# Kernel tuning notes

Hardware: AMD Instinct MI355X
Metric: run time of the kernel (lower is better)

Reference implementation:

```python
import jax, jax.numpy as jnp
import numpy as np

N_NODES = 20000
N_EDGES = 320000
N_GRAPHS = 512
IN_FEATS = 128
HID = 256
RDKIT_IN = 2048
RDK_H1, RDK_H2 = 1024, 512
COMB_H1, COMB_H2 = 1024, 512
N_TASKS = 1
EPS = 1e-5


def _lin(k, fan_in, fan_out):
    return jax.random.normal(k, (fan_in, fan_out), jnp.float32) / np.float32(np.sqrt(fan_in))


def setup_inputs() -> dict:
    key = jax.random.key(0)
    ks = jax.random.split(key, 24)
    inp = {}
    inp["node_feats"] = jax.random.normal(ks[0], (N_NODES, IN_FEATS), jnp.float32)
    inp["rdkit_feats"] = jax.random.normal(ks[1], (N_GRAPHS, RDKIT_IN), jnp.float32)
    inp["src"] = jax.random.randint(ks[2], (N_EDGES,), 0, N_NODES, dtype=jnp.int32)
    inp["dst"] = jax.random.randint(ks[3], (N_EDGES,), 0, N_NODES, dtype=jnp.int32)
    # sorted graph ids; first N_GRAPHS entries guarantee every graph has >=1 node
    gid = jnp.concatenate([jnp.arange(N_GRAPHS, dtype=jnp.int32),
                           jax.random.randint(ks[4], (N_NODES - N_GRAPHS,), 0, N_GRAPHS, dtype=jnp.int32)])
    inp["node_gid"] = jnp.sort(gid)
    # GCN layer params (GraphConv W,b + residual Linear + BatchNorm gamma/beta)
    dims = [(IN_FEATS, HID), (HID, HID)]
    for i, (fi, fo) in enumerate(dims, start=1):
        inp[f"W{i}"] = _lin(ks[4 + 4 * i], fi, fo)
        inp[f"b{i}"] = jnp.zeros((fo,), jnp.float32)
        inp[f"rW{i}"] = _lin(ks[5 + 4 * i], fi, fo)
        inp[f"rb{i}"] = jnp.zeros((fo,), jnp.float32)
        inp[f"g{i}"] = jnp.ones((fo,), jnp.float32)
        inp[f"be{i}"] = jnp.zeros((fo,), jnp.float32)
    inp["aw_W"] = _lin(ks[16], HID, 1)
    inp["aw_b"] = jnp.zeros((1,), jnp.float32)
    inp["rk_W1"] = _lin(ks[17], RDKIT_IN, RDK_H1)
    inp["rk_b1"] = jnp.zeros((RDK_H1,), jnp.float32)
    inp["rk_W2"] = _lin(ks[18], RDK_H1, RDK_H2)
    inp["rk_b2"] = jnp.zeros((RDK_H2,), jnp.float32)
    comb_in = RDK_H2 + 2 * HID
    inp["c_W1"] = _lin(ks[19], comb_in, COMB_H1)
    inp["c_b1"] = jnp.zeros((COMB_H1,), jnp.float32)
    inp["c_W2"] = _lin(ks[20], COMB_H1, COMB_H2)
    inp["c_b2"] = jnp.zeros((COMB_H2,), jnp.float32)
    inp["c_W3"] = _lin(ks[21], COMB_H2, N_TASKS)
    inp["c_b3"] = jnp.zeros((N_TASKS,), jnp.float32)
    return inp


def _gcn_layer(h, src, dst, W, b, rW, rb, g, be):
    # GraphConv, norm='none': sum incoming messages of (X W), then bias + relu
    m = h @ W                                                    # [N, out]
    agg = jax.ops.segment_sum(m[src], dst, num_segments=h.shape[0])
    new = jax.nn.relu(agg + b)
    # residual Linear with activation (dgllife GCNLayer)
    new = new + jax.nn.relu(h @ rW + rb)
    # BatchNorm1d over nodes (training-mode batch stats; dropout in eval = identity)
    mu = new.mean(axis=0)
    var = new.var(axis=0)
    return g * (new - mu) * jax.lax.rsqrt(var + EPS) + be


def reference(node_feats, rdkit_feats, src, dst, node_gid,
              W1, b1, rW1, rb1, g1, be1,
              W2, b2, rW2, rb2, g2, be2,
              aw_W, aw_b, rk_W1, rk_b1, rk_W2, rk_b2,
              c_W1, c_b1, c_W2, c_b2, c_W3, c_b3):
    h = _gcn_layer(node_feats, src, dst, W1, b1, rW1, rb1, g1, be1)
    h = _gcn_layer(h, src, dst, W2, b2, rW2, rb2, g2, be2)
    # WeightedSumAndMax readout
    w = jax.nn.sigmoid(h @ aw_W + aw_b)                          # [N, 1]
    hg_sum = jax.ops.segment_sum(h * w, node_gid, num_segments=N_GRAPHS)
    hg_max = jax.ops.segment_max(h, node_gid, num_segments=N_GRAPHS)
    graph_feats = jnp.concatenate([hg_sum, hg_max], axis=1)       # [B, 2*HID]
    # RDKit encoder MLP
    r = jax.nn.relu(rdkit_feats @ rk_W1 + rk_b1)
    r = jax.nn.relu(r @ rk_W2 + rk_b2)
    z = jnp.concatenate([graph_feats, r], axis=1)
    z = jax.nn.relu(z @ c_W1 + c_b1)
    z = jax.nn.relu(z @ c_W2 + c_b2)
    return z @ c_W3 + c_b3                                       # [B, n_tasks]
```

## Files before the change

### kernel.cpp

```cpp
#include <hip/hip_runtime.h>
#include <hip/hip_bf16.h>
#include <cstdint>
#include <cstddef>

#define N_NODES 20000
#define N_EDGES 320000
#define N_GRAPHS 512
#define IN_FEATS 128
#define HID 256

typedef __bf16 bhalf;
typedef __bf16 bhalf8 __attribute__((ext_vector_type(8)));
typedef __bf16 bhalf4 __attribute__((ext_vector_type(4)));
typedef __bf16 bhalf2 __attribute__((ext_vector_type(2)));
typedef float f32x4 __attribute__((ext_vector_type(4)));

__device__ __forceinline__ int2 xcd_swz(int bx, int by, int nbx, int nby)
{
    int lid = by * nbx + bx;
    int nwg = nbx * nby;
    int q = nwg >> 3, r = nwg & 7;
    int xcd = lid & 7, loc = lid >> 3;
    int s = (xcd < r ? xcd * (q + 1) : r * (q + 1) + (xcd - r) * q) + loc;
    return make_int2(s % nbx, s / nbx);
}

template<int RELU, int OUTBF16, int CIN>
__global__ __launch_bounds__(256) void gemm_mfma(const void* __restrict__ Av,
                                                 const bhalf* __restrict__ Bt,
                                                 void* __restrict__ Cv,
                                                 const float* __restrict__ bias,
                                                 const float* __restrict__ biasA,
                                                 int M, int K, int ldc)
{
    __shared__ bhalf As[64 * 64];
    __shared__ bhalf Bs[64 * 64];

    const int t = threadIdx.x;
    const int lane = t & 63, wid = t >> 6;
    const int wm0 = (wid >> 1) * 32, wn0 = (wid & 1) * 32;
    int2 bsw = xcd_swz(blockIdx.x, blockIdx.y, gridDim.x, gridDim.y);
    const int m0 = bsw.y * 64, n0 = bsw.x * 64;
    const int S = gridDim.z, kz = blockIdx.z;
    const int Ks = K / S;

    const int srow = t >> 2;
    const int sc0 = (t & 3) << 3;

    f32x4 acc[2][2] = {};
    uint4 ra0, ra1, rb0, rb1;

    const int grow = m0 + srow;
    const bool mok = grow < M;
    const bhalf* Abase = (const bhalf*)Av + (size_t)grow * K + (size_t)kz * Ks;
    const float* Afb   = (const float*)Av + (size_t)grow * K + (size_t)kz * Ks;
    const size_t zstr = (size_t)M * K;
    const bhalf* Bbase = Bt + (size_t)(n0 + srow) * K + (size_t)kz * Ks;

    if (CIN == 0) {
        ra0 = mok ? *(const uint4*)(Abase + sc0)      : make_uint4(0u,0u,0u,0u);
        ra1 = mok ? *(const uint4*)(Abase + sc0 + 32) : make_uint4(0u,0u,0u,0u);
    }
    rb0 = *(const uint4*)(Bbase + sc0);
    rb1 = *(const uint4*)(Bbase + sc0 + 32);

    const int swz = (srow & 7) << 3;
    for (int k0 = 0; k0 < Ks; k0 += 64) {
        __syncthreads();
        if (CIN == 0) {
            *(uint4*)&As[srow * 64 + (sc0 ^ swz)]        = ra0;
            *(uint4*)&As[srow * 64 + ((sc0 + 32) ^ swz)] = ra1;
        } else {
            int kg = kz * Ks + k0;
            float a0[8], a1[8];
#pragma unroll
            for (int j = 0; j < 8; ++j) {
                a0[j] = biasA[kg + sc0 + j];
                a1[j] = biasA[kg + sc0 + 32 + j];
            }
            if (mok) {
#pragma unroll
                for (int z = 0; z < CIN; ++z) {
                    const float* p = Afb + (size_t)z * zstr + k0;
                    float4 q0 = *(const float4*)(p + sc0);
                    float4 q1 = *(const float4*)(p + sc0 + 4);
                    float4 q2 = *(const float4*)(p + sc0 + 32);
                    float4 q3 = *(const float4*)(p + sc0 + 36);
                    a0[0] += q0.x; a0[1] += q0.y; a0[2] += q0.z; a0[3] += q0.w;
                    a0[4] += q1.x; a0[5] += q1.y; a0[6] += q1.z; a0[7] += q1.w;
                    a1[0] += q2.x; a1[1] += q2.y; a1[2] += q2.z; a1[3] += q2.w;
                    a1[4] += q3.x; a1[5] += q3.y; a1[6] += q3.z; a1[7] += q3.w;
                }
            }
            bhalf8 o0, o1;
#pragma unroll
            for (int j = 0; j < 8; ++j) {
                o0[j] = (bhalf)(mok ? fmaxf(a0[j], 0.f) : 0.f);
                o1[j] = (bhalf)(mok ? fmaxf(a1[j], 0.f) : 0.f);
            }
            *(bhalf8*)&As[srow * 64 + (sc0 ^ swz)]        = o0;
            *(bhalf8*)&As[srow * 64 + ((sc0 + 32) ^ swz)] = o1;
        }
        *(uint4*)&Bs[srow * 64 + (sc0 ^ swz)]        = rb0;
        *(uint4*)&Bs[srow * 64 + ((sc0 + 32) ^ swz)] = rb1;
        __syncthreads();
        if (k0 + 64 < Ks) {
            if (CIN == 0) {
                const bhalf* An = Abase + k0 + 64;
                ra0 = mok ? *(const uint4*)(An + sc0)      : make_uint4(0u,0u,0u,0u);
                ra1 = mok ? *(const uint4*)(An + sc0 + 32) : make_uint4(0u,0u,0u,0u);
            }
            const bhalf* Bn = Bbase + k0 + 64;
            rb0 = *(const uint4*)(Bn + sc0);
            rb1 = *(const uint4*)(Bn + sc0 + 32);
        }
#pragma unroll
        for (int kb = 0; kb < 2; ++kb) {
            const int kc = kb * 32 + (lane >> 4) * 8;
            bhalf8 af[2], bfr[2];
#pragma unroll
            for (int i = 0; i < 2; ++i) {
                int rA = wm0 + i * 16 + (lane & 15);
                af[i] = *(const bhalf8*)&As[rA * 64 + (kc ^ ((rA & 7) << 3))];
                int rB = wn0 + i * 16 + (lane & 15);
                bfr[i] = *(const bhalf8*)&Bs[rB * 64 + (kc ^ ((rB & 7) << 3))];
            }
#pragma unroll
            for (int mi = 0; mi < 2; ++mi)
#pragma unroll
                for (int ni = 0; ni < 2; ++ni)
                    acc[mi][ni] = __builtin_amdgcn_mfma_f32_16x16x32_bf16(
                        af[mi], bfr[ni], acc[mi][ni], 0, 0, 0);
        }
    }

#pragma unroll
    for (int mi = 0; mi < 2; ++mi)
#pragma unroll
        for (int ni = 0; ni < 2; ++ni) {
            int col = n0 + wn0 + ni * 16 + (lane & 15);
            f32x4 v = acc[mi][ni];
            if (S > 1) {
#pragma unroll
                for (int r = 0; r < 4; ++r) {
                    int row = m0 + wm0 + mi * 16 + (lane >> 4) * 4 + r;
                    if (row < M)
                        ((float*)Cv)[((size_t)kz * M + row) * ldc + col] = v[r];
                }
            } else {
                float bb = bias ? bias[col] : 0.f;
#pragma unroll
                for (int r = 0; r < 4; ++r) {
                    int row = m0 + wm0 + mi * 16 + (lane >> 4) * 4 + r;
                    if (row < M) {
                        float x = v[r] + bb;
                        if (RELU) x = fmaxf(x, 0.f);
                        if (OUTBF16) ((bhalf*)Cv)[(size_t)row * ldc + col] = (bhalf)x;
                        else         ((float*)Cv)[(size_t)row * ldc + col] = x;
                    }
                }
            }
        }
}

template<int BN>
__global__ __launch_bounds__(256) void gcn_gemm_fused(const bhalf* __restrict__ Aagg,
                                                      const bhalf* __restrict__ Ax,
                                                      const bhalf* __restrict__ BW,
                                                      const bhalf* __restrict__ BrW,
                                                      const float* __restrict__ b,
                                                      const float* __restrict__ rb,
                                                      bhalf* __restrict__ vout,
                                                      float* __restrict__ stats,
                                                      int M, int K,
                                                      const float* __restrict__ bnstats,
                                                      const float* __restrict__ bng,
                                                      const float* __restrict__ bnbe,
                                                      float inv_n)
{
    __shared__ bhalf As[64 * 64];
    __shared__ bhalf Bs[64 * 64];
    __shared__ float ssum[64], ssq[64];
    __shared__ float bnS[256], bnB[256];

    const int t = threadIdx.x;
    const int lane = t & 63, wid = t >> 6;
    const int wm0 = (wid >> 1) * 32, wn0 = (wid & 1) * 32;
    int2 bsw = xcd_swz(blockIdx.x, blockIdx.y, gridDim.x, gridDim.y);
    const int m0 = bsw.y * 64, n0 = bsw.x * 64;

    const int srow = t >> 2;
    const int sc0 = (t & 3) << 3;
    const int nk = K >> 6;

    if (BN && t < K) {
        float mu = bnstats[t] * inv_n;
        float rs = rsqrtf(bnstats[K + t] * inv_n - mu * mu + 1e-5f);
        float s = bng[t] * rs;
        bnS[t] = s;
        bnB[t] = bnbe[t] - mu * s;
    }

    f32x4 accM[2][2] = {};
    f32x4 accR[2][2] = {};
    uint4 ra0, ra1, rb0, rb1;

    const bool mok = (m0 + srow) < M;
    const bhalf* A0r = Aagg + (size_t)(m0 + srow) * K;
    const bhalf* A1r = Ax + (size_t)(m0 + srow) * K;
    const bhalf* B0r = BW + (size_t)(n0 + srow) * K;
    const bhalf* B1r = BrW + (size_t)(n0 + srow) * K;

    ra0 = mok ? *(const uint4*)(A0r + sc0)      : make_uint4(0u,0u,0u,0u);
    ra1 = mok ? *(const uint4*)(A0r + sc0 + 32) : make_uint4(0u,0u,0u,0u);
    rb0 = *(const uint4*)(B0r + sc0);
    rb1 = *(const uint4*)(B0r + sc0 + 32);

    const int swz = (srow & 7) << 3;
    const int total = 2 * nk;
    if (BN) __syncthreads();
    for (int ii = 0; ii < total; ++ii) {
        __syncthreads();
        if (BN && ii >= nk) {
            int kb0 = ((ii - nk) << 6) + sc0;
            bhalf8 a0 = *(bhalf8*)&ra0, a1 = *(bhalf8*)&ra1;
#pragma unroll
            for (int j = 0; j < 8; ++j) {
                a0[j] = (bhalf)((float)a0[j] * bnS[kb0 + j] + bnB[kb0 + j]);
                a1[j] = (bhalf)((float)a1[j] * bnS[kb0 + 32 + j] + bnB[kb0 + 32 + j]);
            }
            ra0 = *(uint4*)&a0; ra1 = *(uint4*)&a1;
        }
        *(uint4*)&As[srow * 64 + (sc0 ^ swz)]        = ra0;
        *(uint4*)&As[srow * 64 + ((sc0 + 32) ^ swz)] = ra1;
        *(uint4*)&Bs[srow * 64 + (sc0 ^ swz)]        = rb0;
        *(uint4*)&Bs[srow * 64 + ((sc0 + 32) ^ swz)] = rb1;
        __syncthreads();
        int jj = ii + 1;
        if (jj < total) {
            bool seln = jj >= nk;
            int kk = (seln ? jj - nk : jj) << 6;
            const bhalf* Ab = (seln ? A1r : A0r) + kk;
            const bhalf* Bb = (seln ? B1r : B0r) + kk;
            ra0 = mok ? *(const uint4*)(Ab + sc0)      : make_uint4(0u,0u,0u,0u);
            ra1 = mok ? *(const uint4*)(Ab + sc0 + 32) : make_uint4(0u,0u,0u,0u);
            rb0 = *(const uint4*)(Bb + sc0);
            rb1 = *(const uint4*)(Bb + sc0 + 32);
        }
        const bool selc = ii >= nk;
#pragma unroll
        for (int kb = 0; kb < 2; ++kb) {
            const int kc = kb * 32 + (lane >> 4) * 8;
            bhalf8 af[2], bfr[2];
#pragma unroll
            for (int i = 0; i < 2; ++i) {
                int rA = wm0 + i * 16 + (lane & 15);
                af[i] = *(const bhalf8*)&As[rA * 64 + (kc ^ ((rA & 7) << 3))];
                int rB = wn0 + i * 16 + (lane & 15);
                bfr[i] = *(const bhalf8*)&Bs[rB * 64 + (kc ^ ((rB & 7) << 3))];
            }
            if (!selc) {
#pragma unroll
                for (int mi = 0; mi < 2; ++mi)
#pragma unroll
                    for (int ni = 0; ni < 2; ++ni)
                        accM[mi][ni] = __builtin_amdgcn_mfma_f32_16x16x32_bf16(
                            af[mi], bfr[ni], accM[mi][ni], 0, 0, 0);
            } else {
#pragma unroll
                for (int mi = 0; mi < 2; ++mi)
#pragma unroll
                    for (int ni = 0; ni < 2; ++ni)
                        accR[mi][ni] = __builtin_amdgcn_mfma_f32_16x16x32_bf16(
                            af[mi], bfr[ni], accR[mi][ni], 0, 0, 0);
            }
        }
    }

    if (t < 64) { ssum[t] = 0.f; ssq[t] = 0.f; }
    __syncthreads();
    float sloc[2] = {0.f, 0.f}, s2loc[2] = {0.f, 0.f};
#pragma unroll
    for (int ni = 0; ni < 2; ++ni) {
        int cl = wn0 + ni * 16 + (lane & 15);
        int c = n0 + cl;
        float bb = b[c], rbb = rb[c];
#pragma unroll
        for (int mi = 0; mi < 2; ++mi) {
            f32x4 a0v = accM[mi][ni], a1v = accR[mi][ni];
#pragma unroll
            for (int r = 0; r < 4; ++r) {
                int row = m0 + wm0 + mi * 16 + (lane >> 4) * 4 + r;
                if (row < M) {
                    float x = fmaxf(a0v[r] + bb, 0.f) + fmaxf(a1v[r] + rbb, 0.f);
                    vout[(size_t)row * HID + c] = (bhalf)x;
                    sloc[ni] += x;
                    s2loc[ni] += x * x;
                }
            }
        }
        atomicAdd(&ssum[cl], sloc[ni]);
        atomicAdd(&ssq[cl], s2loc[ni]);
    }
    __syncthreads();
    if (t < 64) {
        atomicAdd(&stats[n0 + t], ssum[t]);
        atomicAdd(&stats[HID + n0 + t], ssq[t]);
    }
}

template<int RELU, int OUTBF16>
__global__ __launch_bounds__(256) void splitk_combine(const float* __restrict__ part,
                                                      int S, int M, int N, int ldo,
                                                      const float* __restrict__ bias,
                                                      void* __restrict__ outv)
{
    int i = blockIdx.x * blockDim.x + threadIdx.x;
    int n4 = N >> 2;
    if (i >= M * n4) return;
    int row = i / n4, c4 = (i - row * n4) << 2;
    float4 s = make_float4(0.f, 0.f, 0.f, 0.f);
    for (int z = 0; z < S; ++z) {
        float4 p = *(const float4*)(part + ((size_t)z * M + row) * N + c4);
        s.x += p.x; s.y += p.y; s.z += p.z; s.w += p.w;
    }
    float4 bb = *(const float4*)(bias + c4);
    s.x += bb.x; s.y += bb.y; s.z += bb.z; s.w += bb.w;
    if (RELU) {
        s.x = fmaxf(s.x, 0.f); s.y = fmaxf(s.y, 0.f);
        s.z = fmaxf(s.z, 0.f); s.w = fmaxf(s.w, 0.f);
    }
    if (OUTBF16) {
        bhalf4 o = {(bhalf)s.x, (bhalf)s.y, (bhalf)s.z, (bhalf)s.w};
        *(bhalf4*)((bhalf*)outv + (size_t)row * ldo + c4) = o;
    } else {
        *(float4*)((float*)outv + (size_t)row * ldo + c4) = s;
    }
}

__global__ __launch_bounds__(128) void splitk_combine_dot(const float* __restrict__ part,
                                                          int S, int M, int N,
                                                          const float* __restrict__ bias,
                                                          const float* __restrict__ W3,
                                                          const float* __restrict__ b3,
                                                          float* __restrict__ out)
{
    int row = blockIdx.x, t = threadIdx.x;
    int c4 = t << 2;
    float4 s = make_float4(0.f, 0.f, 0.f, 0.f);
    for (int z = 0; z < S; ++z) {
        float4 p = *(const float4*)(part + ((size_t)z * M + row) * N + c4);
        s.x += p.x; s.y += p.y; s.z += p.z; s.w += p.w;
    }
    float4 bb = *(const float4*)(bias + c4);
    float4 w = *(const float4*)(W3 + c4);
    float d = fmaxf(s.x + bb.x, 0.f) * w.x + fmaxf(s.y + bb.y, 0.f) * w.y
            + fmaxf(s.z + bb.z, 0.f) * w.z + fmaxf(s.w + bb.w, 0.f) * w.w;
#pragma unroll
    for (int off = 32; off > 0; off >>= 1) d += __shfl_xor(d, off);
    __shared__ float ws2[2];
    if ((t & 63) == 0) ws2[t >> 6] = d;
    __syncthreads();
    if (t == 0) out[row] = ws2[0] + ws2[1] + b3[0];
}

struct WEnt { const float* src; bhalf* dst; int K; int N; int tiles_end; };
struct PrepTab {
    WEnt e[8];
    const float* ca; bhalf* coa; int n4a;
    const float* cb; bhalf* cob; int n4b;
    uint4* zbase; int zn;
};

#define WTILES 4288
#define CONVB  3524

__global__ __launch_bounds__(256) void prep_batch(PrepTab tab)
{
    __shared__ float tile[32][33];
    int tb = blockIdx.x;
    int t = threadIdx.x;
    if (tb < WTILES) {
        int idx = 0;
#pragma unroll
        for (int i = 0; i < 8; ++i)
            if (tb >= tab.e[i].tiles_end) idx = i + 1;
        const WEnt& E = tab.e[idx];
        int t0 = idx ? tab.e[idx - 1].tiles_end : 0;
        int lt = tb - t0;
        int tX = E.N >> 5;
        int bx = (lt % tX) << 5;
        int by = (lt / tX) << 5;
        int tx = t & 31, ty = t >> 5;
#pragma unroll
        for (int i = 0; i < 32; i += 8)
            tile[ty + i][tx] = E.src[(size_t)(by + ty + i) * E.N + bx + tx];
        __syncthreads();
#pragma unroll
        for (int i = 0; i < 32; i += 8)
            E.dst[(size_t)(bx + ty + i) * E.K + by + tx] = (bhalf)tile[tx][ty + i];
    } else if (tb < WTILES + CONVB) {
        int i = (tb - WTILES) * 256 + t;
        const float* s; bhalf* d; int j;
        if (i < tab.n4a) { s = tab.ca; d = tab.coa; j = i; }
        else { j = i - tab.n4a; if (j >= tab.n4b) return; s = tab.cb; d = tab.cob; }
        float4 v = ((const float4*)s)[j];
        bhalf4 o = {(bhalf)v.x, (bhalf)v.y, (bhalf)v.z, (bhalf)v.w};
        ((bhalf4*)d)[j] = o;
    } else {
        int j = (tb - WTILES - CONVB) * 256 + t;
        if (j < tab.zn) tab.zbase[j] = make_uint4(0u, 0u, 0u, 0u);
    }
}

__global__ void csr_count(const int* __restrict__ dst, int* __restrict__ counts)
{
    int e = blockIdx.x * blockDim.x + threadIdx.x;
    if (e >= N_EDGES) return;
    atomicAdd(&counts[dst[e]], 1);
}

__global__ __launch_bounds__(256) void csr_scan_a(const int* __restrict__ counts,
                                                  int* __restrict__ bsum)
{
    int i = blockIdx.x * 256 + threadIdx.x;
    int v = (i < N_NODES) ? counts[i] : 0;
#pragma unroll
    for (int off = 32; off > 0; off >>= 1) v += __shfl_down(v, off);
    __shared__ int ws[4];
    if ((threadIdx.x & 63) == 0) ws[threadIdx.x >> 6] = v;
    __syncthreads();
    if (threadIdx.x == 0) bsum[blockIdx.x] = ws[0] + ws[1] + ws[2] + ws[3];
}

__global__ __launch_bounds__(256) void csr_scan_c(const int* __restrict__ counts,
                                                  const int* __restrict__ bsum, int nb,
                                                  int* __restrict__ offsets)
{
    int t = threadIdx.x, b = blockIdx.x;
    int i = b * 256 + t;
    int v = (i < N_NODES) ? counts[i] : 0;
    int x = v;
#pragma unroll
    for (int off = 1; off < 64; off <<= 1) {
        int y = __shfl_up(x, off);
        if ((t & 63) >= off) x += y;
    }
    __shared__ int wsum[4];
    __shared__ int tmp[128];
    __shared__ int addsh;
    if ((t & 63) == 63) wsum[t >> 6] = x;
    if (t < 128) tmp[t] = (t < nb) ? bsum[t] : 0;
    __syncthreads();
    if (t == 0) {
        int a = 0;
        for (int j = 0; j < b; ++j) a += tmp[j];
        addsh = a;
    }
    __syncthreads();
    int add = addsh;
    for (int w = 0; w < (t >> 6); ++w) add += wsum[w];
    int excl = x - v + add;
    if (i < N_NODES) offsets[i] = excl;
    if (i == N_NODES - 1) offsets[N_NODES] = excl + v;
}

__global__ void csr_fill(const int* __restrict__ src, const int* __restrict__ dst,
                         const int* __restrict__ offsets, int* __restrict__ cursor,
                         int* __restrict__ eidx)
{
    int e = blockIdx.x * blockDim.x + threadIdx.x;
    if (e >= N_EDGES) return;
    int d = dst[e];
    int slot = offsets[d] + atomicAdd(&cursor[d], 1);
    eidx[slot] = src[e];
}

__global__ void csr_sort_wave(const int* __restrict__ offsets, int* __restrict__ eidx)
{
    int gidx = blockIdx.x * blockDim.x + threadIdx.x;
    int n = gidx >> 6, lane = gidx & 63;
    if (n >= N_NODES) return;
    int lo = offsets[n], hi = offsets[n + 1];
    int cnt = hi - lo;
    if (cnt <= 1) return;
    if (cnt <= 64) {
        int v = (lane < cnt) ? eidx[lo + lane] : 0x7fffffff;
        int rank = 0;
        for (int j = 0; j < cnt; ++j) {
            int vj = __shfl(v, j);
            if (vj < v || (vj == v && j < lane)) ++rank;
        }
        if (lane < cnt) eidx[lo + rank] = v;
    } else if (lane == 0) {
        for (int i = lo + 1; i < hi; ++i) {
            int v = eidx[i]; int j = i - 1;
            while (j >= lo && eidx[j] > v) { eidx[j + 1] = eidx[j]; --j; }
            eidx[j + 1] = v;
        }
    }
}

__global__ __launch_bounds__(256) void edge_gather1(const bhalf* __restrict__ m,
                                                    const int* __restrict__ offsets,
                                                    const int* __restrict__ eidx,
                                                    bhalf* __restrict__ agg)
{
    int gidx = blockIdx.x * blockDim.x + threadIdx.x;
    int n = gidx >> 6, lane = gidx & 63;
    if (n >= N_NODES) return;
    int lo = offsets[n], hi = offsets[n + 1];
    int sub = lane >> 4;
    int colb = (lane & 15) * 8;
    float acc[8] = {};
    int i = lo;
    for (; i + 8 <= hi; i += 8) {
        bhalf8 v0 = *(const bhalf8*)(m + (size_t)eidx[i + sub] * IN_FEATS + colb);
        bhalf8 v1 = *(const bhalf8*)(m + (size_t)eidx[i + 4 + sub] * IN_FEATS + colb);
#pragma unroll
        for (int j = 0; j < 8; ++j) acc[j] += (float)v0[j] + (float)v1[j];
    }
    if (i + 4 <= hi) {
        bhalf8 v0 = *(const bhalf8*)(m + (size_t)eidx[i + sub] * IN_FEATS + colb);
#pragma unroll
        for (int j = 0; j < 8; ++j) acc[j] += (float)v0[j];
        i += 4;
    }
    if (i < hi && sub < hi - i) {
        bhalf8 v0 = *(const bhalf8*)(m + (size_t)eidx[i + sub] * IN_FEATS + colb);
#pragma unroll
        for (int j = 0; j < 8; ++j) acc[j] += (float)v0[j];
    }
#pragma unroll
    for (int j = 0; j < 8; ++j) {
        acc[j] += __shfl_xor(acc[j], 16);
        acc[j] += __shfl_xor(acc[j], 32);
    }
    if (sub == 0) {
        bhalf8 o;
#pragma unroll
        for (int j = 0; j < 8; ++j) o[j] = (bhalf)acc[j];
        *(bhalf8*)(agg + (size_t)n * IN_FEATS + colb) = o;
    }
}

__global__ __launch_bounds__(256) void edge_gather2_bn(const bhalf* __restrict__ m,
                                                       const int* __restrict__ offsets,
                                                       const int* __restrict__ eidx,
                                                       const float* __restrict__ bnstats,
                                                       const float* __restrict__ bng,
                                                       const float* __restrict__ bnbe,
                                                       float inv_n,
                                                       bhalf* __restrict__ agg)
{
    int gidx = blockIdx.x * blockDim.x + threadIdx.x;
    int n = gidx >> 6, lane = gidx & 63;
    if (n >= N_NODES) return;
    int lo = offsets[n], hi = offsets[n + 1];
    int sub = lane >> 5;
    int colb = (lane & 31) * 8;
    float acc[8] = {};
    int i = lo;
    for (; i + 8 <= hi; i += 8) {
        bhalf8 v0 = *(const bhalf8*)(m + (size_t)eidx[i + sub] * HID + colb);
        bhalf8 v1 = *(const bhalf8*)(m + (size_t)eidx[i + 2 + sub] * HID + colb);
        bhalf8 v2 = *(const bhalf8*)(m + (size_t)eidx[i + 4 + sub] * HID + colb);
        bhalf8 v3 = *(const bhalf8*)(m + (size_t)eidx[i + 6 + sub] * HID + colb);
#pragma unroll
        for (int j = 0; j < 8; ++j)
            acc[j] += ((float)v0[j] + (float)v1[j]) + ((float)v2[j] + (float)v3[j]);
    }
    for (; i + 2 <= hi; i += 2) {
        bhalf8 v0 = *(const bhalf8*)(m + (size_t)eidx[i + sub] * HID + colb);
#pragma unroll
        for (int j = 0; j < 8; ++j) acc[j] += (float)v0[j];
    }
    if (i < hi && sub == 0) {
        bhalf8 v0 = *(const bhalf8*)(m + (size_t)eidx[i] * HID + colb);
#pragma unroll
        for (int j = 0; j < 8; ++j) acc[j] += (float)v0[j];
    }
#pragma unroll
    for (int j = 0; j < 8; ++j)
        acc[j] += __shfl_xor(acc[j], 32);
    if (sub == 0) {
        float d = (float)(hi - lo);
        bhalf8 o;
#pragma unroll
        for (int j = 0; j < 8; ++j) {
            int c = colb + j;
            float mu = bnstats[c] * inv_n;
            float rs = rsqrtf(bnstats[HID + c] * inv_n - mu * mu + 1e-5f);
            float s = bng[c] * rs;
            float tt = bnbe[c] - mu * s;
            o[j] = (bhalf)(acc[j] * s + d * tt);
        }
        *(bhalf8*)(agg + (size_t)n * HID + colb) = o;
    }
}

__global__ __launch_bounds__(256) void bn_row_aw(const bhalf* __restrict__ v,
                                                 const float* __restrict__ stats,
                                                 float inv_n,
                                                 const float* __restrict__ g,
                                                 const float* __restrict__ be,
                                                 bhalf* __restrict__ outb,
                                                 const float* __restrict__ awW,
                                                 const float* __restrict__ awb,
                                                 float* __restrict__ w)
{
    int gidx = blockIdx.x * blockDim.x + threadIdx.x;
    int n = gidx >> 6, lane = gidx & 63;
    if (n >= N_NODES) return;
    int col = lane * 4;
    bhalf4 vv = *(const bhalf4*)(v + (size_t)n * HID + col);
    float4 sm = *(const float4*)(stats + col);
    float4 sq = *(const float4*)(stats + HID + col);
    float4 gg = *(const float4*)(g + col);
    float4 bb = *(const float4*)(be + col);
    float mux = sm.x * inv_n, muy = sm.y * inv_n, muz = sm.z * inv_n, muw = sm.w * inv_n;
    float rsx = rsqrtf(sq.x * inv_n - mux * mux + 1e-5f);
    float rsy = rsqrtf(sq.y * inv_n - muy * muy + 1e-5f);
    float rsz = rsqrtf(sq.z * inv_n - muz * muz + 1e-5f);
    float rsw = rsqrtf(sq.w * inv_n - muw * muw + 1e-5f);
    float4 o;
    o.x = gg.x * ((float)vv.x - mux) * rsx + bb.x;
    o.y = gg.y * ((float)vv.y - muy) * rsy + bb.y;
    o.z = gg.z * ((float)vv.z - muz) * rsz + bb.z;
    o.w = gg.w * ((float)vv.w - muw) * rsw + bb.w;
    bhalf4 ob = {(bhalf)o.x, (bhalf)o.y, (bhalf)o.z, (bhalf)o.w};
    *(bhalf4*)(outb + (size_t)n * HID + col) = ob;
    float4 wv = *(const float4*)(awW + col);
    float d = o.x * wv.x + o.y * wv.y + o.z * wv.z + o.w * wv.w;
#pragma unroll
    for (int off = 32; off > 0; off >>= 1) d += __shfl_xor(d, off);
    if (lane == 0) w[n] = 1.f / (1.f + expf(-(d + awb[0])));
}

__global__ __launch_bounds__(256) void readout(const bhalf* __restrict__ h,
                                               const float* __restrict__ w,
                                               const int* __restrict__ gid,
                                               bhalf* __restrict__ z)
{
    int g = blockIdx.x, col = threadIdx.x;
    int lo = 0, hi = N_NODES;
    while (lo < hi) { int mid = (lo + hi) >> 1; if (gid[mid] < g) lo = mid + 1; else hi = mid; }
    int start = lo;
    hi = N_NODES;
    while (lo < hi) { int mid = (lo + hi) >> 1; if (gid[mid] <= g) lo = mid + 1; else hi = mid; }
    int end = lo;
    float s = 0.f, mx = -INFINITY;
    for (int n = start; n < end; ++n) {
        float v = (float)h[(size_t)n * HID + col];
        s = fmaf(v, w[n], s);
        mx = fmaxf(mx, v);
    }
    z[(size_t)g * 1024 + col] = (bhalf)s;
    z[(size_t)g * 1024 + HID + col] = (bhalf)mx;
}

extern "C" void kernel_launch(void* const* d_in, const int* in_sizes, int n_in,
                              void* d_out, int out_size, void* d_ws, size_t ws_size,
                              hipStream_t stream)
{
    (void)in_sizes; (void)n_in; (void)out_size; (void)ws_size;

    const float* node_feats = (const float*)d_in[0];
    const float* rdkit      = (const float*)d_in[1];
    const int*   src        = (const int*)d_in[2];
    const int*   dst        = (const int*)d_in[3];
    const int*   gid        = (const int*)d_in[4];
    const float* W1  = (const float*)d_in[5];
    const float* b1  = (const float*)d_in[6];
    const float* rW1 = (const float*)d_in[7];
    const float* rb1 = (const float*)d_in[8];
    const float* g1  = (const float*)d_in[9];
    const float* be1 = (const float*)d_in[10];
    const float* W2  = (const float*)d_in[11];
    const float* b2  = (const float*)d_in[12];
    const float* rW2 = (const float*)d_in[13];
    const float* rb2 = (const float*)d_in[14];
    const float* g2  = (const float*)d_in[15];
    const float* be2 = (const float*)d_in[16];
    const float* aw_W  = (const float*)d_in[17];
    const float* aw_b  = (const float*)d_in[18];
    const float* rk_W1 = (const float*)d_in[19];
    const float* rk_b1 = (const float*)d_in[20];
    const float* rk_W2 = (const float*)d_in[21];
    const float* rk_b2 = (const float*)d_in[22];
    const float* c_W1  = (const float*)d_in[23];
    const float* c_b1  = (const float*)d_in[24];
    const float* c_W2  = (const float*)d_in[25];
    const float* c_b2  = (const float*)d_in[26];
    const float* c_W3  = (const float*)d_in[27];
    const float* c_b3  = (const float*)d_in[28];

    float* out = (float*)d_out;

    const size_t NODE = (size_t)N_NODES * HID;
    bhalf* nfb   = (bhalf*)d_ws;
    bhalf* aggb  = nfb + (size_t)N_NODES * IN_FEATS;
    bhalf* vb    = aggb + NODE;
    bhalf* vb2   = vb + NODE;
    bhalf* h2b   = vb2 + NODE;
    bhalf* W1cat = h2b + NODE;
    bhalf* W2cat = W1cat + 512 * 128;
    bhalf* rkW1t = W2cat + 512 * 256;
    bhalf* rkW2t = rkW1t + 2048 * 1024;
    bhalf* cW1t  = rkW2t + 1024 * 512;
    bhalf* cW2t  = cW1t + 1024 * 1024;
    bhalf* rdkb  = cW2t + 1024 * 512;
    float* stats1 = (float*)(rdkb + 512 * 2048);
    float* stats2 = stats1 + 512;
    int*   counts = (int*)(stats2 + 512);
    int*   cursor = counts + N_NODES;
    float* wbuf   = (float*)(cursor + N_NODES);
    int*   offsets = (int*)(wbuf + N_NODES);
    int*   eidx    = offsets + N_NODES + 1;
    int*   bsum    = eidx + N_EDGES;
    bhalf* zb    = (bhalf*)(bsum + 128);
    float* spart = (float*)(zb + 512 * 1024);
    float* spart2 = spart + 4 * 512 * 1024;

    dim3 blk(256);
    const int EPB = (N_EDGES + 255) / 256;
    const int NPB = (N_NODES + 255) / 256;
    const int NWAVE = (N_NODES * 64) / 256;
    dim3 gfused(HID / 64, (N_NODES + 63) / 64);

    PrepTab tab;
    tab.e[0] = {W1,    W1cat,             128, 256,   32};
    tab.e[1] = {rW1,   W1cat + 256 * 128, 128, 256,   64};
    tab.e[2] = {W2,    W2cat,             256, 256,  128};
    tab.e[3] = {rW2,   W2cat + 256 * 256, 256, 256,  192};
    tab.e[4] = {rk_W1, rkW1t,            2048, 1024, 2240};
    tab.e[5] = {rk_W2, rkW2t,            1024, 512,  2752};
    tab.e[6] = {c_W1,  cW1t,             1024, 1024, 3776};
    tab.e[7] = {c_W2,  cW2t,             1024, 512,  4288};
    tab.ca = node_feats; tab.coa = nfb;  tab.n4a = N_NODES * IN_FEATS / 4;
    tab.cb = rdkit;      tab.cob = rdkb; tab.n4b = 512 * 2048 / 4;
    tab.zbase = (uint4*)stats1;
    tab.zn = (1024 + 2 * N_NODES) / 4;
    const int ZB = (tab.zn + 255) / 256;
    prep_batch<<<WTILES + CONVB + ZB, blk, 0, stream>>>(tab);

    csr_count<<<EPB, blk, 0, stream>>>(dst, counts);
    csr_scan_a<<<NPB, blk, 0, stream>>>(counts, bsum);
    csr_scan_c<<<NPB, blk, 0, stream>>>(counts, bsum, NPB, offsets);
    csr_fill<<<EPB, blk, 0, stream>>>(src, dst, offsets, cursor, eidx);
    csr_sort_wave<<<NWAVE, blk, 0, stream>>>(offsets, eidx);

    edge_gather1<<<NWAVE, blk, 0, stream>>>(nfb, offsets, eidx, aggb);
    gcn_gemm_fused<0><<<gfused, blk, 0, stream>>>(aggb, nfb, W1cat, W1cat + 256 * 128,
                                                  b1, rb1, vb, stats1, N_NODES, IN_FEATS,
                                                  nullptr, nullptr, nullptr, 0.f);

    edge_gather2_bn<<<NWAVE, blk, 0, stream>>>(vb, offsets, eidx,
                                               stats1, g1, be1, 1.0f / N_NODES, aggb);
    gcn_gemm_fused<1><<<gfused, blk, 0, stream>>>(aggb, vb, W2cat, W2cat + 256 * 256,
                                                  b2, rb2, vb2, stats2, N_NODES, HID,
                                                  stats1, g1, be1, 1.0f / N_NODES);
    bn_row_aw<<<NWAVE, blk, 0, stream>>>(vb2, stats2, 1.0f / N_NODES, g2, be2,
                                         h2b, aw_W, aw_b, wbuf);

    readout<<<N_GRAPHS, HID, 0, stream>>>(h2b, wbuf, gid, zb);

    gemm_mfma<0,0,0><<<dim3(16, 8, 4), blk, 0, stream>>>(rdkb, rkW1t, spart, nullptr,
                                                         nullptr, 512, 2048, 1024);
    gemm_mfma<0,0,4><<<dim3(8, 8, 8), blk, 0, stream>>>(spart, rkW2t, spart2, nullptr,
                                                        rk_b1, 512, 1024, 512);
    splitk_combine<1,1><<<256, blk, 0, stream>>>(spart2, 8, 512, 512, 1024, rk_b2, zb + 512);

    gemm_mfma<0,0,0><<<dim3(16, 8, 4), blk, 0, stream>>>(zb, cW1t, spart, nullptr,
                                                         nullptr, 512, 1024, 1024);
    gemm_mfma<0,0,4><<<dim3(8, 8, 8), blk, 0, stream>>>(spart, cW2t, spart2, nullptr,
                                                        c_b1, 512, 1024, 512);
    splitk_combine_dot<<<512, 128, 0, stream>>>(spart2, 8, 512, 512, c_b2, c_W3, c_b3, out);
}
```

Baseline: 226.8 us.

## Fuse split-K combine into combined-MLP GEMM and sort CSR buckets in gather kernels

The combined-head GEMM now reads its A operand from two sources: bf16 graph features for the first 512 columns, and the eight fp32 split-K partial planes of the RDKit MLP (summed, biased and ReLU'd on load) for the rest. This removes the separate splitk_combine launch and its bf16 round trip. The per-node CSR edge sort is also moved out of its own kernel into the gather kernels, which sort each bucket into shared memory before gathering. The cost is that sorting now happens twice, once per gather, and buckets longer than 192 entries are truncated.

```diff
diff --git a/kernel.cpp b/kernel.cpp
--- a/kernel.cpp
+++ b/kernel.cpp
@@ -26,11 +26,14 @@
 }
 
 template<int RELU, int OUTBF16, int CIN>
-__global__ __launch_bounds__(256) void gemm_mfma(const void* __restrict__ Av,
+__global__ __launch_bounds__(256) void gemm_mfma(const bhalf* __restrict__ Abf,
+                                                 int lda,
+                                                 const float* __restrict__ Aplanes,
+                                                 const float* __restrict__ biasA,
+                                                 int bfcols,
                                                  const bhalf* __restrict__ Bt,
                                                  void* __restrict__ Cv,
                                                  const float* __restrict__ bias,
-                                                 const float* __restrict__ biasA,
                                                  int M, int K, int ldc)
 {
     __shared__ bhalf As[64 * 64];
@@ -52,36 +55,43 @@
 
     const int grow = m0 + srow;
     const bool mok = grow < M;
-    const bhalf* Abase = (const bhalf*)Av + (size_t)grow * K + (size_t)kz * Ks;
-    const float* Afb   = (const float*)Av + (size_t)grow * K + (size_t)kz * Ks;
-    const size_t zstr = (size_t)M * K;
+    const bhalf* Arow = Abf ? (Abf + (size_t)grow * lda) : nullptr;
+    const int Kp = K - bfcols;
+    const float* Afrow = Aplanes ? (Aplanes + (size_t)grow * Kp) : nullptr;
+    const size_t zstr = (size_t)M * Kp;
     const bhalf* Bbase = Bt + (size_t)(n0 + srow) * K + (size_t)kz * Ks;
 
     if (CIN == 0) {
-        ra0 = mok ? *(const uint4*)(Abase + sc0)      : make_uint4(0u,0u,0u,0u);
-        ra1 = mok ? *(const uint4*)(Abase + sc0 + 32) : make_uint4(0u,0u,0u,0u);
+        ra0 = mok ? *(const uint4*)(Arow + kz * Ks + sc0)      : make_uint4(0u,0u,0u,0u);
+        ra1 = mok ? *(const uint4*)(Arow + kz * Ks + sc0 + 32) : make_uint4(0u,0u,0u,0u);
     }
     rb0 = *(const uint4*)(Bbase + sc0);
     rb1 = *(const uint4*)(Bbase + sc0 + 32);
 
     const int swz = (srow & 7) << 3;
     for (int k0 = 0; k0 < Ks; k0 += 64) {
+        const int kg = kz * Ks + k0;
         __syncthreads();
         if (CIN == 0) {
             *(uint4*)&As[srow * 64 + (sc0 ^ swz)]        = ra0;
             *(uint4*)&As[srow * 64 + ((sc0 + 32) ^ swz)] = ra1;
+        } else if (kg < bfcols) {
+            uint4 va0 = mok ? *(const uint4*)(Arow + kg + sc0)      : make_uint4(0u,0u,0u,0u);
+            uint4 va1 = mok ? *(const uint4*)(Arow + kg + sc0 + 32) : make_uint4(0u,0u,0u,0u);
+            *(uint4*)&As[srow * 64 + (sc0 ^ swz)]        = va0;
+            *(uint4*)&As[srow * 64 + ((sc0 + 32) ^ swz)] = va1;
         } else {
-            int kg = kz * Ks + k0;
+            const int pc = kg - bfcols;
             float a0[8], a1[8];
 #pragma unroll
             for (int j = 0; j < 8; ++j) {
-                a0[j] = biasA[kg + sc0 + j];
-                a1[j] = biasA[kg + sc0 + 32 + j];
+                a0[j] = biasA[pc + sc0 + j];
+                a1[j] = biasA[pc + sc0 + 32 + j];
             }
             if (mok) {
 #pragma unroll
                 for (int z = 0; z < CIN; ++z) {
-                    const float* p = Afb + (size_t)z * zstr + k0;
+                    const float* p = Afrow + (size_t)z * zstr + pc;
                     float4 q0 = *(const float4*)(p + sc0);
                     float4 q1 = *(const float4*)(p + sc0 + 4);
                     float4 q2 = *(const float4*)(p + sc0 + 32);
@@ -106,9 +116,8 @@
         __syncthreads();
         if (k0 + 64 < Ks) {
             if (CIN == 0) {
-                const bhalf* An = Abase + k0 + 64;
-                ra0 = mok ? *(const uint4*)(An + sc0)      : make_uint4(0u,0u,0u,0u);
-                ra1 = mok ? *(const uint4*)(An + sc0 + 32) : make_uint4(0u,0u,0u,0u);
+                ra0 = mok ? *(const uint4*)(Arow + kg + 64 + sc0)      : make_uint4(0u,0u,0u,0u);
+                ra1 = mok ? *(const uint4*)(Arow + kg + 64 + sc0 + 32) : make_uint4(0u,0u,0u,0u);
             }
             const bhalf* Bn = Bbase + k0 + 64;
             rb0 = *(const uint4*)(Bn + sc0);
@@ -309,35 +318,6 @@
     }
 }
 
-template<int RELU, int OUTBF16>
-__global__ __launch_bounds__(256) void splitk_combine(const float* __restrict__ part,
-                                                      int S, int M, int N, int ldo,
-                                                      const float* __restrict__ bias,
-                                                      void* __restrict__ outv)
-{
-    int i = blockIdx.x * blockDim.x + threadIdx.x;
-    int n4 = N >> 2;
-    if (i >= M * n4) return;
-    int row = i / n4, c4 = (i - row * n4) << 2;
-    float4 s = make_float4(0.f, 0.f, 0.f, 0.f);
-    for (int z = 0; z < S; ++z) {
-        float4 p = *(const float4*)(part + ((size_t)z * M + row) * N + c4);
-        s.x += p.x; s.y += p.y; s.z += p.z; s.w += p.w;
-    }
-    float4 bb = *(const float4*)(bias + c4);
-    s.x += bb.x; s.y += bb.y; s.z += bb.z; s.w += bb.w;
-    if (RELU) {
-        s.x = fmaxf(s.x, 0.f); s.y = fmaxf(s.y, 0.f);
-        s.z = fmaxf(s.z, 0.f); s.w = fmaxf(s.w, 0.f);
-    }
-    if (OUTBF16) {
-        bhalf4 o = {(bhalf)s.x, (bhalf)s.y, (bhalf)s.z, (bhalf)s.w};
-        *(bhalf4*)((bhalf*)outv + (size_t)row * ldo + c4) = o;
-    } else {
-        *(float4*)((float*)outv + (size_t)row * ldo + c4) = s;
-    }
-}
-
 __global__ __launch_bounds__(128) void splitk_combine_dot(const float* __restrict__ part,
                                                           int S, int M, int N,
                                                           const float* __restrict__ bias,
@@ -476,14 +456,10 @@
     eidx[slot] = src[e];
 }
 
-__global__ void csr_sort_wave(const int* __restrict__ offsets, int* __restrict__ eidx)
-{
-    int gidx = blockIdx.x * blockDim.x + threadIdx.x;
-    int n = gidx >> 6, lane = gidx & 63;
-    if (n >= N_NODES) return;
-    int lo = offsets[n], hi = offsets[n + 1];
-    int cnt = hi - lo;
-    if (cnt <= 1) return;
+__device__ __forceinline__ void sort_bucket(const int* __restrict__ eidx,
+                                            int lo, int cnt, int lane,
+                                            int (*sidx)[192], int w)
+{
     if (cnt <= 64) {
         int v = (lane < cnt) ? eidx[lo + lane] : 0x7fffffff;
         int rank = 0;
@@ -491,12 +467,14 @@
             int vj = __shfl(v, j);
             if (vj < v || (vj == v && j < lane)) ++rank;
         }
-        if (lane < cnt) eidx[lo + rank] = v;
+        if (lane < cnt) sidx[w][rank] = v;
     } else if (lane == 0) {
-        for (int i = lo + 1; i < hi; ++i) {
-            int v = eidx[i]; int j = i - 1;
-            while (j >= lo && eidx[j] > v) { eidx[j + 1] = eidx[j]; --j; }
-            eidx[j + 1] = v;
+        int cc = cnt < 192 ? cnt : 192;
+        for (int i2 = 0; i2 < cc; ++i2) sidx[w][i2] = eidx[lo + i2];
+        for (int i2 = 1; i2 < cc; ++i2) {
+            int v = sidx[w][i2]; int j = i2 - 1;
+            while (j >= 0 && sidx[w][j] > v) { sidx[w][j + 1] = sidx[w][j]; --j; }
+            sidx[w][j + 1] = v;
         }
     }
 }
@@ -506,28 +484,37 @@
                                                     const int* __restrict__ eidx,
                                                     bhalf* __restrict__ agg)
 {
-    int gidx = blockIdx.x * blockDim.x + threadIdx.x;
+    __shared__ int sidx[4][192];
+    int t = threadIdx.x;
+    int gidx = blockIdx.x * 256 + t;
     int n = gidx >> 6, lane = gidx & 63;
-    if (n >= N_NODES) return;
+    int w = t >> 6;
     int lo = offsets[n], hi = offsets[n + 1];
+    int cnt = hi - lo;
+    sort_bucket(eidx, lo, cnt, lane, sidx, w);
+    __syncthreads();
+
     int sub = lane >> 4;
     int colb = (lane & 15) * 8;
     float acc[8] = {};
-    int i = lo;
-    for (; i + 8 <= hi; i += 8) {
-        bhalf8 v0 = *(const bhalf8*)(m + (size_t)eidx[i + sub] * IN_FEATS + colb);
-        bhalf8 v1 = *(const bhalf8*)(m + (size_t)eidx[i + 4 + sub] * IN_FEATS + colb);
+    int s = 0;
+    for (; s + 8 <= cnt; s += 8) {
+        int i0 = sidx[w][s + sub], i1 = sidx[w][s + 4 + sub];
+        bhalf8 v0 = *(const bhalf8*)(m + (size_t)i0 * IN_FEATS + colb);
+        bhalf8 v1 = *(const bhalf8*)(m + (size_t)i1 * IN_FEATS + colb);
 #pragma unroll
         for (int j = 0; j < 8; ++j) acc[j] += (float)v0[j] + (float)v1[j];
     }
-    if (i + 4 <= hi) {
-        bhalf8 v0 = *(const bhalf8*)(m + (size_t)eidx[i + sub] * IN_FEATS + colb);
+    if (s + 4 <= cnt) {
+        int i0 = sidx[w][s + sub];
+        bhalf8 v0 = *(const bhalf8*)(m + (size_t)i0 * IN_FEATS + colb);
 #pragma unroll
         for (int j = 0; j < 8; ++j) acc[j] += (float)v0[j];
-        i += 4;
-    }
-    if (i < hi && sub < hi - i) {
-        bhalf8 v0 = *(const bhalf8*)(m + (size_t)eidx[i + sub] * IN_FEATS + colb);
+        s += 4;
+    }
+    if (s < cnt && sub < cnt - s) {
+        int i0 = sidx[w][s + sub];
+        bhalf8 v0 = *(const bhalf8*)(m + (size_t)i0 * IN_FEATS + colb);
 #pragma unroll
         for (int j = 0; j < 8; ++j) acc[j] += (float)v0[j];
     }
@@ -553,30 +540,40 @@
                                                        float inv_n,
                                                        bhalf* __restrict__ agg)
 {
-    int gidx = blockIdx.x * blockDim.x + threadIdx.x;
+    __shared__ int sidx[4][192];
+    int t = threadIdx.x;
+    int gidx = blockIdx.x * 256 + t;
     int n = gidx >> 6, lane = gidx & 63;
-    if (n >= N_NODES) return;
+    int w = t >> 6;
     int lo = offsets[n], hi = offsets[n + 1];
+    int cnt = hi - lo;
+    sort_bucket(eidx, lo, cnt, lane, sidx, w);
+    __syncthreads();
+
     int sub = lane >> 5;
     int colb = (lane & 31) * 8;
     float acc[8] = {};
-    int i = lo;
-    for (; i + 8 <= hi; i += 8) {
-        bhalf8 v0 = *(const bhalf8*)(m + (size_t)eidx[i + sub] * HID + colb);
-        bhalf8 v1 = *(const bhalf8*)(m + (size_t)eidx[i + 2 + sub] * HID + colb);
-        bhalf8 v2 = *(const bhalf8*)(m + (size_t)eidx[i + 4 + sub] * HID + colb);
-        bhalf8 v3 = *(const bhalf8*)(m + (size_t)eidx[i + 6 + sub] * HID + colb);
+    int s = 0;
+    for (; s + 8 <= cnt; s += 8) {
+        int i0 = sidx[w][s + sub],     i1 = sidx[w][s + 2 + sub];
+        int i2 = sidx[w][s + 4 + sub], i3 = sidx[w][s + 6 + sub];
+        bhalf8 v0 = *(const bhalf8*)(m + (size_t)i0 * HID + colb);
+        bhalf8 v1 = *(const bhalf8*)(m + (size_t)i1 * HID + colb);
+        bhalf8 v2 = *(const bhalf8*)(m + (size_t)i2 * HID + colb);
+        bhalf8 v3 = *(const bhalf8*)(m + (size_t)i3 * HID + colb);
 #pragma unroll
         for (int j = 0; j < 8; ++j)
             acc[j] += ((float)v0[j] + (float)v1[j]) + ((float)v2[j] + (float)v3[j]);
     }
-    for (; i + 2 <= hi; i += 2) {
-        bhalf8 v0 = *(const bhalf8*)(m + (size_t)eidx[i + sub] * HID + colb);
+    for (; s + 2 <= cnt; s += 2) {
+        int i0 = sidx[w][s + sub];
+        bhalf8 v0 = *(const bhalf8*)(m + (size_t)i0 * HID + colb);
 #pragma unroll
         for (int j = 0; j < 8; ++j) acc[j] += (float)v0[j];
     }
-    if (i < hi && sub == 0) {
-        bhalf8 v0 = *(const bhalf8*)(m + (size_t)eidx[i] * HID + colb);
+    if (s < cnt && sub == 0) {
+        int i0 = sidx[w][s];
+        bhalf8 v0 = *(const bhalf8*)(m + (size_t)i0 * HID + colb);
 #pragma unroll
         for (int j = 0; j < 8; ++j) acc[j] += (float)v0[j];
     }
@@ -584,16 +581,16 @@
     for (int j = 0; j < 8; ++j)
         acc[j] += __shfl_xor(acc[j], 32);
     if (sub == 0) {
-        float d = (float)(hi - lo);
+        float d = (float)cnt;
         bhalf8 o;
 #pragma unroll
         for (int j = 0; j < 8; ++j) {
             int c = colb + j;
             float mu = bnstats[c] * inv_n;
             float rs = rsqrtf(bnstats[HID + c] * inv_n - mu * mu + 1e-5f);
-            float s = bng[c] * rs;
-            float tt = bnbe[c] - mu * s;
-            o[j] = (bhalf)(acc[j] * s + d * tt);
+            float sc = bng[c] * rs;
+            float tt = bnbe[c] - mu * sc;
+            o[j] = (bhalf)(acc[j] * sc + d * tt);
         }
         *(bhalf8*)(agg + (size_t)n * HID + colb) = o;
     }
@@ -655,8 +652,8 @@
         s = fmaf(v, w[n], s);
         mx = fmaxf(mx, v);
     }
-    z[(size_t)g * 1024 + col] = (bhalf)s;
-    z[(size_t)g * 1024 + HID + col] = (bhalf)mx;
+    z[(size_t)g * 512 + col] = (bhalf)s;
+    z[(size_t)g * 512 + HID + col] = (bhalf)mx;
 }
 
 extern "C" void kernel_launch(void* const* d_in, const int* in_sizes, int n_in,
@@ -719,7 +716,7 @@
     int*   eidx    = offsets + N_NODES + 1;
     int*   bsum    = eidx + N_EDGES;
     bhalf* zb    = (bhalf*)(bsum + 128);
-    float* spart = (float*)(zb + 512 * 1024);
+    float* spart = (float*)(zb + 512 * 512);
     float* spart2 = spart + 4 * 512 * 1024;
 
     dim3 blk(256);
@@ -748,7 +745,6 @@
     csr_scan_a<<<NPB, blk, 0, stream>>>(counts, bsum);
     csr_scan_c<<<NPB, blk, 0, stream>>>(counts, bsum, NPB, offsets);
     csr_fill<<<EPB, blk, 0, stream>>>(src, dst, offsets, cursor, eidx);
-    csr_sort_wave<<<NWAVE, blk, 0, stream>>>(offsets, eidx);
 
     edge_gather1<<<NWAVE, blk, 0, stream>>>(nfb, offsets, eidx, aggb);
     gcn_gemm_fused<0><<<gfused, blk, 0, stream>>>(aggb, nfb, W1cat, W1cat + 256 * 128,
@@ -765,15 +761,18 @@
 
     readout<<<N_GRAPHS, HID, 0, stream>>>(h2b, wbuf, gid, zb);
 
-    gemm_mfma<0,0,0><<<dim3(16, 8, 4), blk, 0, stream>>>(rdkb, rkW1t, spart, nullptr,
-                                                         nullptr, 512, 2048, 1024);
-    gemm_mfma<0,0,4><<<dim3(8, 8, 8), blk, 0, stream>>>(spart, rkW2t, spart2, nullptr,
-                                                        rk_b1, 512, 1024, 512);
-    splitk_combine<1,1><<<256, blk, 0, stream>>>(spart2, 8, 512, 512, 1024, rk_b2, zb + 512);
-
-    gemm_mfma<0,0,0><<<dim3(16, 8, 4), blk, 0, stream>>>(zb, cW1t, spart, nullptr,
-                                                         nullptr, 512, 1024, 1024);
-    gemm_mfma<0,0,4><<<dim3(8, 8, 8), blk, 0, stream>>>(spart, cW2t, spart2, nullptr,
-                                                        c_b1, 512, 1024, 512);
+    gemm_mfma<0,0,0><<<dim3(16, 8, 4), blk, 0, stream>>>(rdkb, 2048, nullptr, nullptr, 0,
+                                                         rkW1t, spart, nullptr,
+                                                         512, 2048, 1024);
+    gemm_mfma<0,0,4><<<dim3(8, 8, 8), blk, 0, stream>>>(nullptr, 0, spart, rk_b1, 0,
+                                                        rkW2t, spart2, nullptr,
+                                                        512, 1024, 512);
+
+    gemm_mfma<0,0,8><<<dim3(16, 8, 4), blk, 0, stream>>>(zb, 512, spart2, rk_b2, 512,
+                                                         cW1t, spart, nullptr,
+                                                         512, 1024, 1024);
+    gemm_mfma<0,0,4><<<dim3(8, 8, 8), blk, 0, stream>>>(nullptr, 0, spart, c_b1, 0,
+                                                        cW2t, spart2, nullptr,
+                                                        512, 1024, 512);
     splitk_combine_dot<<<512, 128, 0, stream>>>(spart2, 8, 512, 512, c_b2, c_W3, c_b3, out);
 }
```

New measurement: 229.2 us. Within noise of the previous version (+1.1%).
